# Kernel optimization log

Measured on AMD Instinct MI355X. Metric: run time of the kernel, lower is better.

Reference implementation:

```python
import jax, jax.numpy as jnp
import numpy as np

LN_EPS = 1e-5

def setup_inputs() -> dict:
    key = jax.random.key(0)
    ks = jax.random.split(key, 6)
    B, L, F, D, S, C = 64, 4096, 28, 128, 64, 10
    return {
        "x": jax.random.normal(ks[0], (B, 1, L, F), dtype=jnp.float32),
        "W_in": jax.random.normal(ks[1], (D, F), dtype=jnp.float32) * 0.05,
        "b_in": jnp.zeros((D,), dtype=jnp.float32),
        "A": jax.random.normal(ks[2], (S, S), dtype=jnp.float32) * 0.01,
        "Bm": jax.random.normal(ks[3], (S, D), dtype=jnp.float32) * 0.01,
        "Cm": jax.random.normal(ks[4], (D, S), dtype=jnp.float32) * 0.01,
        "ln_g": jnp.ones((D,), dtype=jnp.float32),
        "ln_b": jnp.zeros((D,), dtype=jnp.float32),
        "W_fc": jax.random.normal(ks[5], (C, D), dtype=jnp.float32) * 0.05,
        "b_fc": jnp.zeros((C,), dtype=jnp.float32),
    }

def reference(x, W_in, b_in, A, Bm, Cm, ln_g, ln_b, W_fc, b_fc):
    # x: (B, 1, L, 28) -> (B, L, 28)
    x = jnp.squeeze(x, axis=1)
    # input projection: (B, L, D)
    u = jnp.einsum('blf,df->bld', x, W_in) + b_in
    # precompute B @ u_t for all t: (L, B, S)
    Bu = jnp.einsum('bld,sd->lbs', u, Bm)
    Bdim = x.shape[0]
    S = A.shape[0]
    init_state = jnp.zeros((Bdim, S), dtype=x.dtype)

    def step(state, bu_t):
        new_state = state @ A.T + bu_t  # (B, S)
        return new_state, new_state

    _, states = jax.lax.scan(step, init_state, Bu)  # (L, B, S)
    # output projection: (B, L, D)
    y = jnp.einsum('lbs,ds->bld', states, Cm)
    # GELU (exact, matches torch nn.GELU default) then LayerNorm over D
    y = jax.nn.gelu(y, approximate=False)
    mean = jnp.mean(y, axis=-1, keepdims=True)
    var = jnp.var(y, axis=-1, keepdims=True)
    y = (y - mean) * jax.lax.rsqrt(var + LN_EPS) * ln_g + ln_b
    # AdaptiveAvgPool1d(1) over time -> (B, D)
    pooled = jnp.mean(y, axis=1)
    logits = pooled @ W_fc.T + b_fc  # (B, n_classes)
    return logits
```

## Files before the change

kernel.cpp:

```cpp
#include <hip/hip_runtime.h>
#include <math.h>

#define B_SZ 64
#define L_SZ 4096
#define F_SZ 28
#define D_SZ 128
#define S_SZ 64
#define C_SZ 10

#define J_TAPS 8
#define KF 29
#define KP 32
#define CL 128
#define NCH (L_SZ / CL)
#define XROWS (CL + J_TAPS - 1)
#define XS 32

#define XSWZ(rt, s) (((s) ^ (((rt) >> 1) & 3)) * 8)

#define SCALE_W 2097152.0f
#define INV_W   (1.0f / 2097152.0f)

#define WS_T_BYTE 32768

typedef _Float16 half8 __attribute__((ext_vector_type(8)));
typedef float    f32x4 __attribute__((ext_vector_type(4)));
typedef float    f32x2 __attribute__((ext_vector_type(2)));

__device__ __forceinline__ float dpp_add16(float v) {
    int x = __float_as_int(v);
    v += __int_as_float(__builtin_amdgcn_update_dpp(0, x, 0xB1, 0xF, 0xF, true));
    x = __float_as_int(v);
    v += __int_as_float(__builtin_amdgcn_update_dpp(0, x, 0x4E, 0xF, 0xF, true));
    x = __float_as_int(v);
    v += __int_as_float(__builtin_amdgcn_update_dpp(0, x, 0x141, 0xF, 0xF, true));
    x = __float_as_int(v);
    v += __int_as_float(__builtin_amdgcn_update_dpp(0, x, 0x140, 0xF, 0xF, true));
    return v;
}

__global__ void __launch_bounds__(256)
prep_kernel(const float* __restrict__ Bm,
            const float* __restrict__ W_in,
            const float* __restrict__ b_in,
            const float* __restrict__ A,
            const float* __restrict__ Cm,
            _Float16* __restrict__ Tf16,
            float* __restrict__ pool_ws) {
    __shared__ float A_lds[S_SZ * S_SZ];
    __shared__ float V[J_TAPS][S_SZ];

    const int tid = threadIdx.x;
    const int f = blockIdx.x;

    for (int idx = f * 256 + tid; idx < B_SZ * D_SZ; idx += KF * 256)
        pool_ws[idx] = 0.f;
    if (f < 3)
        for (int idx = tid; idx < J_TAPS * D_SZ; idx += 256)
            Tf16[idx * KP + KF + f] = (_Float16)0.f;

    for (int i = tid * 4; i < S_SZ * S_SZ; i += 1024)
        *(float4*)(A_lds + i) = *(const float4*)(A + i);

    {
        const int s = tid >> 2, dq = tid & 3;
        const float* bm = Bm + s * D_SZ + dq * 32;
        float acc = 0.f;
        if (f < F_SZ) {
            const float* wi = W_in + (dq * 32) * F_SZ + f;
#pragma unroll
            for (int d = 0; d < 32; ++d) acc = fmaf(bm[d], wi[d * F_SZ], acc);
        } else {
            const float* bi = b_in + dq * 32;
#pragma unroll
            for (int d = 0; d < 32; ++d) acc = fmaf(bm[d], bi[d], acc);
        }
        acc += __shfl_xor(acc, 1);
        acc += __shfl_xor(acc, 2);
        if (dq == 0) V[0][s] = acc;
    }
    __syncthreads();

    for (int j = 1; j < J_TAPS; ++j) {
        const int s = tid >> 2, kq = tid & 3;
        const float* ar = A_lds + s * S_SZ + kq * 16;
        const float* vp = V[j - 1] + kq * 16;
        float acc = 0.f;
#pragma unroll
        for (int k = 0; k < 16; ++k) acc = fmaf(ar[k], vp[k], acc);
        acc += __shfl_xor(acc, 1);
        acc += __shfl_xor(acc, 2);
        if (kq == 0) V[j][s] = acc;
        __syncthreads();
    }

    if (tid < D_SZ) {
        const int d = tid;
        float crow[S_SZ];
#pragma unroll
        for (int i = 0; i < 16; ++i) {
            float4 v = *(const float4*)(Cm + d * S_SZ + 4 * i);
            crow[4*i+0] = v.x; crow[4*i+1] = v.y; crow[4*i+2] = v.z; crow[4*i+3] = v.w;
        }
#pragma unroll
        for (int j = 0; j < J_TAPS; ++j) {
            float acc = 0.f;
#pragma unroll
            for (int s = 0; s < S_SZ; ++s) acc = fmaf(crow[s], V[j][s], acc);
            Tf16[(j * D_SZ + d) * KP + f] = (_Float16)(acc * SCALE_W);
        }
    }
}

__global__ void __launch_bounds__(256, 3)
main_kernel(const float* __restrict__ x,
            const _Float16* __restrict__ Tf16,
            float* __restrict__ pool_ws) {
    __shared__ __align__(16) _Float16 xh[XROWS * XS];

    const int tid  = threadIdx.x;
    const int w    = tid >> 6;
    const int wt   = w >> 1;
    const int wd   = w & 1;
    const int col  = tid & 15;
    const int quad = (tid & 63) >> 4;
    const int ch = blockIdx.x;
    const int b  = blockIdx.y;

    {
        const float* xbase = x + ((size_t)b * L_SZ + ch * CL - (J_TAPS - 1)) * F_SZ;
        for (int task = tid; task < XROWS * 4; task += 256) {
            const int rt = task >> 2, g = task & 3;
            half8 h = (half8){0, 0, 0, 0, 0, 0, 0, 0};
            if (!(ch == 0 && rt < J_TAPS - 1)) {
                const float* s0 = xbase + rt * F_SZ + g * 8;
                float4 v0 = *(const float4*)s0;
                h[0] = (_Float16)v0.x; h[1] = (_Float16)v0.y;
                h[2] = (_Float16)v0.z; h[3] = (_Float16)v0.w;
                if (g < 3) {
                    float4 v1 = *(const float4*)(s0 + 4);
                    h[4] = (_Float16)v1.x; h[5] = (_Float16)v1.y;
                    h[6] = (_Float16)v1.z; h[7] = (_Float16)v1.w;
                } else {
                    h[4] = (_Float16)1.f;
                }
            }
            *(half8*)(xh + rt * XS + XSWZ(rt, g)) = h;
        }
    }
    __syncthreads();

    f32x4 acc[4][4];
#pragma unroll
    for (int tb = 0; tb < 4; ++tb)
#pragma unroll
        for (int db = 0; db < 4; ++db) acc[tb][db] = (f32x4){0.f, 0.f, 0.f, 0.f};

    const _Float16* tp = Tf16 + ((wd * 64 + col) * KP + quad * 8);

#pragma unroll
    for (int j = 0; j < J_TAPS; ++j) {
        half8 bfj[4];
#pragma unroll
        for (int db = 0; db < 4; ++db)
            bfj[db] = *(const half8*)(tp + (j * D_SZ + db * 16) * KP);
#pragma unroll
        for (int tb = 0; tb < 4; ++tb) {
            const int rt = (wt * 4 + tb) * 16 + col + (J_TAPS - 1) - j;
            half8 af = *(const half8*)(xh + rt * XS + XSWZ(rt, quad));
            acc[tb][0] = __builtin_amdgcn_mfma_f32_16x16x32_f16(af, bfj[0], acc[tb][0], 0, 0, 0);
            acc[tb][1] = __builtin_amdgcn_mfma_f32_16x16x32_f16(af, bfj[1], acc[tb][1], 0, 0, 0);
            acc[tb][2] = __builtin_amdgcn_mfma_f32_16x16x32_f16(af, bfj[2], acc[tb][2], 0, 0, 0);
            acc[tb][3] = __builtin_amdgcn_mfma_f32_16x16x32_f16(af, bfj[3], acc[tb][3], 0, 0, 0);
        }
    }

#pragma unroll
    for (int tb = 0; tb < 4; ++tb)
#pragma unroll
        for (int db = 0; db < 4; ++db) {
            f32x4 a  = acc[tb][db];
            f32x4 bb = a * (0.5f * INV_W);
            f32x4 b2 = bb * bb;
            f32x4 P  = b2 * (-0.3039579415628160f) + 0.6383076486422944f;
            P = b2 * P + (-1.0638460810704872f);
            P = b2 * P + 1.5957691216057308f;
            acc[tb][db] = b2 * P + bb;
        }

    float* pls = (float*)xh;
    __syncthreads();
#pragma unroll
    for (int tb = 0; tb < 4; ++tb) {
        f32x4 g0 = acc[tb][0], g1 = acc[tb][1], g2 = acc[tb][2], g3 = acc[tb][3];
        f32x4 sv = (g0 + g1) + (g2 + g3);
        f32x4 qv = g0 * g0;
        qv = g1 * g1 + qv;
        qv = g2 * g2 + qv;
        qv = g3 * g3 + qv;
        const int tbase = (wt * 4 + tb) * 16 + quad * 4;
#pragma unroll
        for (int r = 0; r < 4; ++r) {
            float s = dpp_add16(sv[r]);
            float q = dpp_add16(qv[r]);
            if (col == 0)
                *(f32x2*)(pls + (tbase + r) * 4 + wd * 2) = (f32x2){s, q};
        }
    }
    __syncthreads();

    f32x4 poolv[4];
#pragma unroll
    for (int db = 0; db < 4; ++db) poolv[db] = (f32x4){0.f, 0.f, 0.f, 0.f};
    float mr = 0.f;
#pragma unroll
    for (int tb = 0; tb < 4; ++tb) {
        const int tbase = (wt * 4 + tb) * 16 + quad * 4;
        f32x4 rstd4;
#pragma unroll
        for (int r = 0; r < 4; ++r) {
            f32x4 pq = *(const f32x4*)(pls + (tbase + r) * 4);
            float s = pq[0] + pq[2];
            float q = pq[1] + pq[3];
            float mean = s * (1.0f / 128.0f);
            float var  = q * (1.0f / 128.0f) - mean * mean;
            float rstd = 1.0f / sqrtf(var + 1e-5f);
            mr = fmaf(mean, rstd, mr);
            rstd4[r] = rstd;
        }
#pragma unroll
        for (int db = 0; db < 4; ++db)
            poolv[db] = poolv[db] + acc[tb][db] * rstd4;
    }

    float* pp = pls + CL * 4;
#pragma unroll
    for (int db = 0; db < 4; ++db) {
        float vd = (poolv[db][0] + poolv[db][1]) + (poolv[db][2] + poolv[db][3]);
        vd -= mr;
        vd += __shfl_xor(vd, 16);
        vd += __shfl_xor(vd, 32);
        if (quad == 0) pp[w * 64 + db * 16 + col] = vd;
    }
    __syncthreads();
    if (tid < D_SZ) {
        const int dl = tid & 63, dh = tid >> 6;
        atomicAdd(&pool_ws[b * D_SZ + tid],
                  pp[dh * 64 + dl] + pp[(2 + dh) * 64 + dl]);
    }
}

__global__ void __launch_bounds__(64)
head_kernel(const float* __restrict__ pool_ws,
            const float* __restrict__ ln_g,
            const float* __restrict__ ln_b,
            const float* __restrict__ W_fc,
            const float* __restrict__ b_fc,
            float* __restrict__ out) {
    const int b = blockIdx.x;
    const int lane = threadIdx.x;
    const float inv_l = 1.0f / (float)L_SZ;

    float p0 = fmaf(ln_g[lane] * pool_ws[b * D_SZ + lane], inv_l, ln_b[lane]);
    float p1 = fmaf(ln_g[lane + 64] * pool_ws[b * D_SZ + lane + 64], inv_l, ln_b[lane + 64]);

#pragma unroll
    for (int c = 0; c < C_SZ; ++c) {
        float acc = fmaf(p0, W_fc[c * D_SZ + lane], p1 * W_fc[c * D_SZ + lane + 64]);
#pragma unroll
        for (int m = 1; m < 64; m <<= 1) acc += __shfl_xor(acc, m);
        if (lane == 0) out[b * C_SZ + c] = acc + b_fc[c];
    }
}

extern "C" void kernel_launch(void* const* d_in, const int* in_sizes, int n_in,
                              void* d_out, int out_size, void* d_ws, size_t ws_size,
                              hipStream_t stream) {
    const float* x    = (const float*)d_in[0];
    const float* W_in = (const float*)d_in[1];
    const float* b_in = (const float*)d_in[2];
    const float* A    = (const float*)d_in[3];
    const float* Bm   = (const float*)d_in[4];
    const float* Cm   = (const float*)d_in[5];
    const float* ln_g = (const float*)d_in[6];
    const float* ln_b = (const float*)d_in[7];
    const float* W_fc = (const float*)d_in[8];
    const float* b_fc = (const float*)d_in[9];
    float* out = (float*)d_out;

    float*    pool_ws = (float*)d_ws;
    _Float16* Tf16    = (_Float16*)((char*)d_ws + WS_T_BYTE);

    prep_kernel<<<KF, 256, 0, stream>>>(Bm, W_in, b_in, A, Cm, Tf16, pool_ws);
    main_kernel<<<dim3(NCH, B_SZ), 256, 0, stream>>>(x, Tf16, pool_ws);
    head_kernel<<<B_SZ, 64, 0, stream>>>(pool_ws, ln_g, ln_b, W_fc, b_fc, out);
}
```

Before: 132.3 us.

## Split waves over D only, prefetch tap weights, atomically add pooled sums

The block's four waves now each take a 32-wide slice of D across all 128 timesteps, where before they used a 2x2 split over time and D. Each wave therefore reads 8 A fragments from LDS per tap and only 2 B fragments from global memory, and the next tap's B fragments are prefetched with double buffering. The per-row LayerNorm partial sums are combined from four wave partials, and each wave atomically adds its pooled values straight to global memory, which removes one LDS staging step and a barrier. In exchange, LDS A-fragment reads and global atomics per block go up.

```diff
diff --git a/kernel.cpp b/kernel.cpp
--- a/kernel.cpp
+++ b/kernel.cpp
@@ -119,9 +119,7 @@
     __shared__ __align__(16) _Float16 xh[XROWS * XS];
 
     const int tid  = threadIdx.x;
-    const int w    = tid >> 6;
-    const int wt   = w >> 1;
-    const int wd   = w & 1;
+    const int wd   = tid >> 6;
     const int col  = tid & 15;
     const int quad = (tid & 63) >> 4;
     const int ch = blockIdx.x;
@@ -150,35 +148,40 @@
     }
     __syncthreads();
 
-    f32x4 acc[4][4];
-#pragma unroll
-    for (int tb = 0; tb < 4; ++tb)
-#pragma unroll
-        for (int db = 0; db < 4; ++db) acc[tb][db] = (f32x4){0.f, 0.f, 0.f, 0.f};
-
-    const _Float16* tp = Tf16 + ((wd * 64 + col) * KP + quad * 8);
-
+    f32x4 acc[8][2];
+#pragma unroll
+    for (int tb = 0; tb < 8; ++tb) {
+        acc[tb][0] = (f32x4){0.f, 0.f, 0.f, 0.f};
+        acc[tb][1] = (f32x4){0.f, 0.f, 0.f, 0.f};
+    }
+
+    const _Float16* tp = Tf16 + ((wd * 32 + col) * KP + quad * 8);
+
+    half8 bfa0 = *(const half8*)(tp);
+    half8 bfa1 = *(const half8*)(tp + 16 * KP);
+    half8 bfb0, bfb1;
 #pragma unroll
     for (int j = 0; j < J_TAPS; ++j) {
-        half8 bfj[4];
-#pragma unroll
-        for (int db = 0; db < 4; ++db)
-            bfj[db] = *(const half8*)(tp + (j * D_SZ + db * 16) * KP);
-#pragma unroll
-        for (int tb = 0; tb < 4; ++tb) {
-            const int rt = (wt * 4 + tb) * 16 + col + (J_TAPS - 1) - j;
+        half8 c0, c1;
+        if (j & 1) { c0 = bfb0; c1 = bfb1; } else { c0 = bfa0; c1 = bfa1; }
+        if (j < J_TAPS - 1) {
+            const _Float16* tn = tp + (j + 1) * D_SZ * KP;
+            if (j & 1) { bfa0 = *(const half8*)tn; bfa1 = *(const half8*)(tn + 16 * KP); }
+            else       { bfb0 = *(const half8*)tn; bfb1 = *(const half8*)(tn + 16 * KP); }
+        }
+#pragma unroll
+        for (int tb = 0; tb < 8; ++tb) {
+            const int rt = tb * 16 + col + (J_TAPS - 1) - j;
             half8 af = *(const half8*)(xh + rt * XS + XSWZ(rt, quad));
-            acc[tb][0] = __builtin_amdgcn_mfma_f32_16x16x32_f16(af, bfj[0], acc[tb][0], 0, 0, 0);
-            acc[tb][1] = __builtin_amdgcn_mfma_f32_16x16x32_f16(af, bfj[1], acc[tb][1], 0, 0, 0);
-            acc[tb][2] = __builtin_amdgcn_mfma_f32_16x16x32_f16(af, bfj[2], acc[tb][2], 0, 0, 0);
-            acc[tb][3] = __builtin_amdgcn_mfma_f32_16x16x32_f16(af, bfj[3], acc[tb][3], 0, 0, 0);
-        }
-    }
-
-#pragma unroll
-    for (int tb = 0; tb < 4; ++tb)
-#pragma unroll
-        for (int db = 0; db < 4; ++db) {
+            acc[tb][0] = __builtin_amdgcn_mfma_f32_16x16x32_f16(af, c0, acc[tb][0], 0, 0, 0);
+            acc[tb][1] = __builtin_amdgcn_mfma_f32_16x16x32_f16(af, c1, acc[tb][1], 0, 0, 0);
+        }
+    }
+
+#pragma unroll
+    for (int tb = 0; tb < 8; ++tb)
+#pragma unroll
+        for (int db = 0; db < 2; ++db) {
             f32x4 a  = acc[tb][db];
             f32x4 bb = a * (0.5f * INV_W);
             f32x4 b2 = bb * bb;
@@ -191,62 +194,54 @@
     float* pls = (float*)xh;
     __syncthreads();
 #pragma unroll
-    for (int tb = 0; tb < 4; ++tb) {
-        f32x4 g0 = acc[tb][0], g1 = acc[tb][1], g2 = acc[tb][2], g3 = acc[tb][3];
-        f32x4 sv = (g0 + g1) + (g2 + g3);
+    for (int tb = 0; tb < 8; ++tb) {
+        f32x4 g0 = acc[tb][0], g1 = acc[tb][1];
+        f32x4 sv = g0 + g1;
         f32x4 qv = g0 * g0;
         qv = g1 * g1 + qv;
-        qv = g2 * g2 + qv;
-        qv = g3 * g3 + qv;
-        const int tbase = (wt * 4 + tb) * 16 + quad * 4;
+        const int tbase = tb * 16 + quad * 4;
 #pragma unroll
         for (int r = 0; r < 4; ++r) {
             float s = dpp_add16(sv[r]);
             float q = dpp_add16(qv[r]);
             if (col == 0)
-                *(f32x2*)(pls + (tbase + r) * 4 + wd * 2) = (f32x2){s, q};
-        }
-    }
-    __syncthreads();
-
-    f32x4 poolv[4];
-#pragma unroll
-    for (int db = 0; db < 4; ++db) poolv[db] = (f32x4){0.f, 0.f, 0.f, 0.f};
+                *(f32x2*)(pls + (tbase + r) * 8 + wd * 2) = (f32x2){s, q};
+        }
+    }
+    __syncthreads();
+
+    f32x4 poolv[2];
+    poolv[0] = (f32x4){0.f, 0.f, 0.f, 0.f};
+    poolv[1] = (f32x4){0.f, 0.f, 0.f, 0.f};
     float mr = 0.f;
 #pragma unroll
-    for (int tb = 0; tb < 4; ++tb) {
-        const int tbase = (wt * 4 + tb) * 16 + quad * 4;
+    for (int tb = 0; tb < 8; ++tb) {
+        const int tbase = tb * 16 + quad * 4;
         f32x4 rstd4;
 #pragma unroll
         for (int r = 0; r < 4; ++r) {
-            f32x4 pq = *(const f32x4*)(pls + (tbase + r) * 4);
-            float s = pq[0] + pq[2];
-            float q = pq[1] + pq[3];
+            f32x4 p0 = *(const f32x4*)(pls + (tbase + r) * 8);
+            f32x4 p1 = *(const f32x4*)(pls + (tbase + r) * 8 + 4);
+            float s = (p0[0] + p0[2]) + (p1[0] + p1[2]);
+            float q = (p0[1] + p0[3]) + (p1[1] + p1[3]);
             float mean = s * (1.0f / 128.0f);
             float var  = q * (1.0f / 128.0f) - mean * mean;
-            float rstd = 1.0f / sqrtf(var + 1e-5f);
+            float rstd = rsqrtf(var + 1e-5f);
             mr = fmaf(mean, rstd, mr);
             rstd4[r] = rstd;
         }
-#pragma unroll
-        for (int db = 0; db < 4; ++db)
-            poolv[db] = poolv[db] + acc[tb][db] * rstd4;
-    }
-
-    float* pp = pls + CL * 4;
-#pragma unroll
-    for (int db = 0; db < 4; ++db) {
+        poolv[0] = poolv[0] + acc[tb][0] * rstd4;
+        poolv[1] = poolv[1] + acc[tb][1] * rstd4;
+    }
+
+#pragma unroll
+    for (int db = 0; db < 2; ++db) {
         float vd = (poolv[db][0] + poolv[db][1]) + (poolv[db][2] + poolv[db][3]);
         vd -= mr;
         vd += __shfl_xor(vd, 16);
         vd += __shfl_xor(vd, 32);
-        if (quad == 0) pp[w * 64 + db * 16 + col] = vd;
-    }
-    __syncthreads();
-    if (tid < D_SZ) {
-        const int dl = tid & 63, dh = tid >> 6;
-        atomicAdd(&pool_ws[b * D_SZ + tid],
-                  pp[dh * 64 + dl] + pp[(2 + dh) * 64 + dl]);
+        if (quad == 0)
+            atomicAdd(&pool_ws[b * D_SZ + wd * 32 + db * 16 + col], vd);
     }
 }
 
```

Result: no change. 132.6 us (+0.3%).
